# Optimization experiments

Hardware: AMD Instinct MI355X
Metric: run time of the kernel (lower is better)

The kernel has to match this reference:

```python
import jax, jax.numpy as jnp
import numpy as np

B = 4096          # graphs (frames)
NPG = 22          # players per frame
N = B * NPG       # total nodes
E = B * NPG * (NPG - 1)
D_BB = 256        # backbone_dout == GRNN hidden
D_NODE = 128      # raw node feature dim
D_PROJ = 256      # cfg.proj_dout
D_GIN = 64        # glob_din
D_GOUT = 128      # cfg.glob_dout
D_IN = D_BB + D_PROJ  # GRNN input dim = 512


def setup_inputs() -> dict:
    key = jax.random.key(0)
    ks = jax.random.split(key, 24)
    def w(k, shape):
        return jax.random.normal(k, shape, jnp.float32) * 0.05
    inp = {
        "z": jax.random.normal(ks[0], (N, D_BB), jnp.float32),
        "u": jax.random.normal(ks[1], (B, D_GIN), jnp.float32),
        "x": jax.random.normal(ks[2], (N, D_NODE), jnp.float32),
        # edge_index is unused math-wise because GConvGRU is built with K=1 ChebConvs
        "edge_index": jax.random.randint(ks[3], (2, E), 0, N, dtype=jnp.int32),
        "batch": jnp.repeat(jnp.arange(B, dtype=jnp.int32), NPG),
        "batch_size": B,
        "prev_h": jax.random.normal(ks[4], (N, D_BB), jnp.float32),
        # fusion params
        "w_proj": w(ks[5], (D_NODE, D_PROJ)), "b_proj": jnp.zeros((D_PROJ,), jnp.float32),
        "w_glob": w(ks[6], (D_GIN, D_GOUT)), "b_glob": jnp.zeros((D_GOUT,), jnp.float32),
        # GConvGRU (K=1 ChebConv == linear) gate params: update z, reset r, candidate h
        "W_xz": w(ks[7], (D_IN, D_BB)),  "b_xz": jnp.zeros((D_BB,), jnp.float32),
        "W_hz": w(ks[8], (D_BB, D_BB)),  "b_hz": jnp.zeros((D_BB,), jnp.float32),
        "W_xr": w(ks[9], (D_IN, D_BB)),  "b_xr": jnp.zeros((D_BB,), jnp.float32),
        "W_hr": w(ks[10], (D_BB, D_BB)), "b_hr": jnp.zeros((D_BB,), jnp.float32),
        "W_xh": w(ks[11], (D_IN, D_BB)), "b_xh": jnp.zeros((D_BB,), jnp.float32),
        "W_hh": w(ks[12], (D_BB, D_BB)), "b_hh": jnp.zeros((D_BB,), jnp.float32),
    }
    return inp


def reference(z, u, x, edge_index, batch, batch_size, prev_h,
              w_proj, b_proj, w_glob, b_glob,
              W_xz, b_xz, W_hz, b_hz,
              W_xr, b_xr, W_hr, b_hr,
              W_xh, b_xh, W_hh, b_hh):
    # --- GraphGlobalFusion: mean readout + relu(Linear(u)) + concat ---
    sums = jax.ops.segment_sum(z, batch, num_segments=batch_size)            # [B, D_BB]
    cnts = jax.ops.segment_sum(jnp.ones((z.shape[0], 1), z.dtype), batch,
                               num_segments=batch_size)                      # [B, 1]
    graph_emb = sums / jnp.maximum(cnts, 1.0)
    glob_emb = jax.nn.relu(u @ w_glob + b_glob)                              # [B, D_GOUT]
    fused = jnp.concatenate([graph_emb, glob_emb], axis=-1)                  # [B, D_BB+D_GOUT]

    # --- node mode: raw feature projection, then GConvGRU (K=1 -> linear gates) ---
    x_proj = jax.nn.relu(x @ w_proj + b_proj)                                # [N, D_PROJ]
    xin = jnp.concatenate([z, x_proj], axis=-1)                              # [N, D_IN]
    Z = jax.nn.sigmoid(xin @ W_xz + b_xz + prev_h @ W_hz + b_hz)
    R = jax.nn.sigmoid(xin @ W_xr + b_xr + prev_h @ W_hr + b_hr)
    H_tilde = jnp.tanh(xin @ W_xh + b_xh + (prev_h * R) @ W_hh + b_hh)
    h = Z * prev_h + (1.0 - Z) * H_tilde                                     # [N, D_BB]
    return (fused, h)
```

## Files before the change

### kernel.cpp

```cpp
#include <hip/hip_runtime.h>
#include <hip/hip_bf16.h>

#define NNODES 90112
#define BGRAPH 4096
#define NPG 22
#define DBB 256
#define DNODE 128
#define DPROJ 256
#define DGIN 64
#define DGOUT 128

#define WTG_OFF   32768
#define WTHH_OFF  622592
#define WS_BF16_ELEMS 688128

typedef __attribute__((ext_vector_type(8))) short bf16x8;
typedef __attribute__((ext_vector_type(4))) short bf16x4;
typedef __attribute__((ext_vector_type(4))) float f32x4;
typedef __attribute__((ext_vector_type(2))) float f32x2;

__device__ __forceinline__ short f2bf(float f) {
  __hip_bfloat16 h = __float2bfloat16(f);
  return *reinterpret_cast<short*>(&h);
}
__device__ __forceinline__ float bf2f(short s) {
  union { unsigned int u; float f; } c;
  c.u = ((unsigned int)(unsigned short)s) << 16;
  return c.f;
}
__device__ __forceinline__ float fsig(float xv) {
  return __fdividef(1.0f, 1.0f + __expf(-xv));
}
__device__ __forceinline__ float ftanh(float xv) {
  return 1.0f - __fdividef(2.0f, __expf(2.0f * xv) + 1.0f);
}

#define DMA16(gsrc, ldst)                                                        \
  __builtin_amdgcn_global_load_lds(                                              \
      (const __attribute__((address_space(1))) void*)(gsrc),                     \
      (__attribute__((address_space(3))) void*)(ldst), 16, 0, 0)

template<int N>
__device__ __forceinline__ void vmwaitN() {
  static_assert(N >= 0 && N <= 6, "vmcnt range");
  if constexpr (N == 0) asm volatile("s_waitcnt vmcnt(0)" ::: "memory");
  else if constexpr (N == 1) asm volatile("s_waitcnt vmcnt(1)" ::: "memory");
  else if constexpr (N == 2) asm volatile("s_waitcnt vmcnt(2)" ::: "memory");
  else if constexpr (N == 3) asm volatile("s_waitcnt vmcnt(3)" ::: "memory");
  else if constexpr (N == 4) asm volatile("s_waitcnt vmcnt(4)" ::: "memory");
  else if constexpr (N == 5) asm volatile("s_waitcnt vmcnt(5)" ::: "memory");
  else asm volatile("s_waitcnt vmcnt(6)" ::: "memory");
  __builtin_amdgcn_sched_barrier(0);
}
#define LBAR() do { asm volatile("s_waitcnt lgkmcnt(0)" ::: "memory");           \
                    __builtin_amdgcn_s_barrier(); } while (0)

__global__ void pack_weights(const float* __restrict__ w_proj,
                             const float* __restrict__ W_xz, const float* __restrict__ W_hz,
                             const float* __restrict__ W_xr, const float* __restrict__ W_hr,
                             const float* __restrict__ W_xh, const float* __restrict__ W_hh,
                             const float* __restrict__ b_xz, const float* __restrict__ b_hz,
                             const float* __restrict__ b_xr, const float* __restrict__ b_hr,
                             const float* __restrict__ b_xh, const float* __restrict__ b_hh,
                             __hip_bfloat16* __restrict__ wsb, float* __restrict__ wsf) {
  int i = blockIdx.x * 256 + threadIdx.x;
  if (i < 32768) {
    int c = i >> 7, k = i & 127;
    wsb[i] = __float2bfloat16(w_proj[k * DPROJ + c]);
  } else if (i < WTHH_OFF) {
    int j = i - WTG_OFF;
    int kc  = j / 24576;
    int rem = j - kc * 24576;
    int ct  = rem >> 9;
    int q   = rem & 511;
    int l   = q >> 3, e = q & 7;
    int l15 = l & 15, kg = l >> 4;
    int k   = kc * 32 + kg * 8 + e;
    int g   = ct >> 4;
    int c   = (ct & 15) * 16 + l15;
    float v;
    if (g == 0)      v = (k < 512) ? W_xz[k * 256 + c] : W_hz[(k - 512) * 256 + c];
    else if (g == 1) v = (k < 512) ? W_xr[k * 256 + c] : W_hr[(k - 512) * 256 + c];
    else             v = (k < 512) ? W_xh[k * 256 + c] : 0.0f;
    wsb[i] = __float2bfloat16(v);
  } else if (i < WS_BF16_ELEMS) {
    int j = i - WTHH_OFF;
    int kc  = j >> 13;
    int rem = j & 8191;
    int ct  = rem >> 9;
    int q   = rem & 511;
    int l   = q >> 3, e = q & 7;
    int l15 = l & 15, kg = l >> 4;
    int k   = kc * 32 + kg * 8 + e;
    int c   = ct * 16 + l15;
    wsb[i] = __float2bfloat16(W_hh[k * 256 + c]);
  }
  if (i < 256) {
    wsf[i]       = b_xz[i] + b_hz[i];
    wsf[256 + i] = b_xr[i] + b_hr[i];
    wsf[512 + i] = b_xh[i] + b_hh[i];
  }
}

__global__ void fused_head(const float* __restrict__ z, const float* __restrict__ u,
                           const float* __restrict__ w_glob, const float* __restrict__ b_glob,
                           float* __restrict__ out) {
  int b = blockIdx.x;
  int t = threadIdx.x;
  __shared__ float us[DGIN];
  if (t < DGIN) us[t] = u[b * DGIN + t];
  __syncthreads();
  const float* zb = z + (size_t)b * NPG * DBB;
  #pragma unroll
  for (int half = 0; half < 2; ++half) {
    int c = t + half * 128;
    float s = 0.f;
    #pragma unroll
    for (int r = 0; r < NPG; ++r) s += zb[r * DBB + c];
    out[(size_t)b * 384 + c] = s * (1.0f / NPG);
  }
  float acc = b_glob[t];
  #pragma unroll
  for (int k = 0; k < DGIN; ++k) acc += us[k] * w_glob[k * DGOUT + t];
  out[(size_t)b * 384 + 256 + t] = fmaxf(acc, 0.f);
}

#define MFMA16(a, b, c) __builtin_amdgcn_mfma_f32_16x16x32_bf16(a, b, c, 0, 0, 0)

template<int KC>
__device__ __forceinline__ void gstep(
    const float* __restrict__ z, const float* __restrict__ prev_h,
    const __hip_bfloat16* __restrict__ wpk,
    __hip_bfloat16* Wb, __hip_bfloat16* ActC, __hip_bfloat16* XP,
    int tid, int r0, int l15, int lg, int wid, int lane,
    f32x4 (&accz)[4], f32x4 (&accr)[4], f32x4 (&acch)[4]) {
  constexpr int  KN       = KC + 1;
  constexpr bool S        = (KN >= 1 && KN <= 7) || (KN >= 16 && KN <= 23);
  constexpr bool BAR      = (KC >= 1 && KC <= 7) || (KC >= 15 && KC <= 23);
  constexpr bool staged   = (KC < 8) || (KC >= 16);
  constexpr bool has_h    = (KC < 16);
  constexpr int  sB       = (KC < 23) ? ((KN < 16) ? 3 : 2) : 0;
  constexpr int  NW       = sB + (S ? 1 : 0);

  f32x2 sl;
  const int srow = tid >> 4, sc2 = (tid & 15) * 2;
  if constexpr (S) {
    const float* src = (KN < 8) ? z : prev_h;
    constexpr int kofs = (KN < 8 ? KN : KN - 16) * 32;
    sl = *(const f32x2*)(src + (size_t)(r0 + srow) * DBB + kofs + sc2);
  }
  if constexpr (BAR) LBAR();

  bf16x8 act[4];
  #pragma unroll
  for (int rt = 0; rt < 4; ++rt) {
    const int row = rt * 16 + l15;
    if constexpr (staged)
      act[rt] = *(const bf16x8*)&ActC[(KC % 3) * 2560 + row * 40 + lg * 8];
    else {
      const int gk = (KC - 8) * 4 + lg;
      act[rt] = *(const bf16x8*)&XP[row * 256 + ((gk ^ (row & 7)) * 8)];
    }
  }

  vmwaitN<NW>();
  bf16x8 wz = *(const bf16x8*)&Wb[((KC & 1) * 3 + 0) * 8192 + wid * 512 + lane * 8];
  bf16x8 wr = *(const bf16x8*)&Wb[((KC & 1) * 3 + 1) * 8192 + wid * 512 + lane * 8];
  bf16x8 wh;
  if constexpr (has_h)
    wh = *(const bf16x8*)&Wb[((KC & 1) * 3 + 2) * 8192 + wid * 512 + lane * 8];

  __builtin_amdgcn_s_setprio(1);
  #pragma unroll
  for (int rt = 0; rt < 4; ++rt) {
    accz[rt] = MFMA16(wz, act[rt], accz[rt]);
    accr[rt] = MFMA16(wr, act[rt], accr[rt]);
    if constexpr (has_h) acch[rt] = MFMA16(wh, act[rt], acch[rt]);
  }
  __builtin_amdgcn_s_setprio(0);

  if constexpr (KC + 2 <= 23) {
    constexpr int ns = ((KC + 2) < 16) ? 3 : 2;
    #pragma unroll
    for (int g = 0; g < 3; ++g)
      if (g < ns)
        DMA16(wpk + (((size_t)(KC + 2) * 48 + g * 16 + wid) * 64 + lane) * 8,
              Wb + (((KC + 2) & 1) * 3 + g) * 8192 + wid * 512);
  }

  if constexpr (S) {
    unsigned int pk = (unsigned int)(unsigned short)f2bf(sl[0]) |
                      ((unsigned int)(unsigned short)f2bf(sl[1]) << 16);
    *(unsigned int*)&ActC[(KN % 3) * 2560 + srow * 40 + sc2] = pk;
  }
}

template<int S>
__device__ __forceinline__ void hstep(
    const __hip_bfloat16* __restrict__ hpk, __hip_bfloat16* Wb, __hip_bfloat16* XP,
    int l15, int lg, int wid, int lane, f32x4 (&acch)[4]) {
  constexpr int NW = (S <= 5) ? 2 : (S == 6) ? 1 : 0;
  bf16x8 act[4];
  #pragma unroll
  for (int rt = 0; rt < 4; ++rt) {
    const int row = rt * 16 + l15;
    const int gk = S * 4 + lg;
    act[rt] = *(const bf16x8*)&XP[row * 256 + ((gk ^ (row & 7)) * 8)];
  }
  vmwaitN<NW>();
  bf16x8 w = *(const bf16x8*)&Wb[(S % 4) * 8192 + wid * 512 + lane * 8];
  __builtin_amdgcn_s_setprio(1);
  #pragma unroll
  for (int rt = 0; rt < 4; ++rt) acch[rt] = MFMA16(w, act[rt], acch[rt]);
  __builtin_amdgcn_s_setprio(0);
  if constexpr (S + 3 <= 7)
    DMA16(hpk + (((size_t)(S + 3) * 16 + wid) * 64 + lane) * 8,
          Wb + ((S + 3) % 4) * 8192 + wid * 512);
}

__global__ __launch_bounds__(1024, 4)
void grnn_main(const float* __restrict__ z, const float* __restrict__ x,
               const float* __restrict__ prev_h, const float* __restrict__ b_proj,
               const __hip_bfloat16* __restrict__ wsb, const float* __restrict__ wsf,
               float* __restrict__ h_out) {
  __shared__ __align__(16) __hip_bfloat16 Wb[6 * 8192];
  __shared__ __align__(16) __hip_bfloat16 Xs[64 * 128];
  __shared__ __align__(16) __hip_bfloat16 XP[64 * 256];
  __shared__ __align__(16) __hip_bfloat16 ActC[3 * 2560];

  const int r0   = blockIdx.x * 64;
  const int tid  = threadIdx.x;
  const int wid  = tid >> 6;
  const int lane = tid & 63;
  const int l15  = lane & 15;
  const int lg   = lane >> 4;
  const int c0   = wid * 16;
  const int cgrp = (c0 >> 3) + (lg >> 1);
  const int lgl  = (lg & 1) * 4;

  const __hip_bfloat16* wpk = wsb + WTG_OFF;
  const __hip_bfloat16* hpk = wsb + WTHH_OFF;

  {
    int row = tid >> 4, c8 = tid & 15;
    const float* p = x + (size_t)(r0 + row) * DNODE + c8 * 8;
    f32x4 f0 = *(const f32x4*)p;
    f32x4 f1 = *(const f32x4*)(p + 4);
    bf16x8 o;
    o[0]=f2bf(f0[0]); o[1]=f2bf(f0[1]); o[2]=f2bf(f0[2]); o[3]=f2bf(f0[3]);
    o[4]=f2bf(f1[0]); o[5]=f2bf(f1[1]); o[6]=f2bf(f1[2]); o[7]=f2bf(f1[3]);
    *(bf16x8*)&Xs[row * 128 + (c8 ^ (row & 7)) * 8] = o;
  }
  __syncthreads();

  f32x2 sl0;
  {
    int row = tid >> 4, c2 = (tid & 15) * 2;
    sl0 = *(const f32x2*)(z + (size_t)(r0 + row) * DBB + c2);
  }
  f32x4 accp[4] = {};
  {
    const __hip_bfloat16* wp0 = wsb + (size_t)(c0 + l15) * DNODE + lg * 8;
    #pragma unroll
    for (int kb = 0; kb < 4; ++kb) {
      bf16x8 wp = *(const bf16x8*)(wp0 + kb * 32);
      const int gk = kb * 4 + lg;
      bf16x8 act[4];
      #pragma unroll
      for (int rt = 0; rt < 4; ++rt) {
        const int row = rt * 16 + l15;
        act[rt] = *(const bf16x8*)&Xs[row * 128 + (gk ^ (row & 7)) * 8];
      }
      __builtin_amdgcn_s_setprio(1);
      #pragma unroll
      for (int rt = 0; rt < 4; ++rt)
        accp[rt] = MFMA16(wp, act[rt], accp[rt]);
      __builtin_amdgcn_s_setprio(0);
    }
  }
  #pragma unroll
  for (int c = 0; c < 2; ++c)
    #pragma unroll
    for (int g = 0; g < 3; ++g)
      DMA16(wpk + (((size_t)c * 48 + g * 16 + wid) * 64 + lane) * 8,
            Wb + ((c & 1) * 3 + g) * 8192 + wid * 512);
  {
    int row = tid >> 4, c2 = (tid & 15) * 2;
    unsigned int pk = (unsigned int)(unsigned short)f2bf(sl0[0]) |
                      ((unsigned int)(unsigned short)f2bf(sl0[1]) << 16);
    *(unsigned int*)&ActC[0 * 2560 + row * 40 + c2] = pk;
  }
  {
    float4 bp4 = *(const float4*)&b_proj[c0 + lg * 4];
    #pragma unroll
    for (int rt = 0; rt < 4; ++rt) {
      int r = rt * 16 + l15;
      bf16x4 o;
      o[0] = f2bf(fmaxf(accp[rt][0] + bp4.x, 0.f));
      o[1] = f2bf(fmaxf(accp[rt][1] + bp4.y, 0.f));
      o[2] = f2bf(fmaxf(accp[rt][2] + bp4.z, 0.f));
      o[3] = f2bf(fmaxf(accp[rt][3] + bp4.w, 0.f));
      *(bf16x4*)&XP[r * 256 + ((cgrp ^ (r & 7)) * 8) + lgl] = o;
    }
  }
  LBAR();

  f32x4 accz[4] = {}, accr[4] = {}, acch[4] = {};
  #define GS(K) gstep<K>(z, prev_h, wpk, Wb, ActC, XP, tid, r0, l15, lg, wid, lane, accz, accr, acch)
  GS(0);  GS(1);  GS(2);  GS(3);  GS(4);  GS(5);  GS(6);  GS(7);
  GS(8);  GS(9);  GS(10); GS(11); GS(12); GS(13); GS(14); GS(15);
  GS(16); GS(17); GS(18); GS(19); GS(20); GS(21); GS(22); GS(23);
  #undef GS

  #pragma unroll
  for (int s = 0; s < 3; ++s)
    DMA16(hpk + (((size_t)s * 16 + wid) * 64 + lane) * 8, Wb + (s % 4) * 8192 + wid * 512);
  f32x4 phv[4];
  {
    float4 br4 = *(const float4*)&wsf[256 + c0 + lg * 4];
    #pragma unroll
    for (int rt = 0; rt < 4; ++rt) {
      int r = rt * 16 + l15;
      phv[rt] = *(const f32x4*)&prev_h[(size_t)(r0 + r) * DBB + c0 + lg * 4];
      bf16x4 o;
      o[0] = f2bf(phv[rt][0] * fsig(accr[rt][0] + br4.x));
      o[1] = f2bf(phv[rt][1] * fsig(accr[rt][1] + br4.y));
      o[2] = f2bf(phv[rt][2] * fsig(accr[rt][2] + br4.z));
      o[3] = f2bf(phv[rt][3] * fsig(accr[rt][3] + br4.w));
      *(bf16x4*)&XP[r * 256 + ((cgrp ^ (r & 7)) * 8) + lgl] = o;
    }
  }
  LBAR();

  #define HS(S) hstep<S>(hpk, Wb, XP, l15, lg, wid, lane, acch)
  HS(0); HS(1); HS(2); HS(3); HS(4); HS(5); HS(6); HS(7);
  #undef HS

  {
    float4 bz4 = *(const float4*)&wsf[c0 + lg * 4];
    float4 bh4 = *(const float4*)&wsf[512 + c0 + lg * 4];
    #pragma unroll
    for (int rt = 0; rt < 4; ++rt) {
      int r = rt * 16 + l15;
      f32x4 hv;
      float zg = fsig(accz[rt][0] + bz4.x);
      hv[0] = zg * phv[rt][0] + (1.f - zg) * ftanh(acch[rt][0] + bh4.x);
      zg = fsig(accz[rt][1] + bz4.y);
      hv[1] = zg * phv[rt][1] + (1.f - zg) * ftanh(acch[rt][1] + bh4.y);
      zg = fsig(accz[rt][2] + bz4.z);
      hv[2] = zg * phv[rt][2] + (1.f - zg) * ftanh(acch[rt][2] + bh4.z);
      zg = fsig(accz[rt][3] + bz4.w);
      hv[3] = zg * phv[rt][3] + (1.f - zg) * ftanh(acch[rt][3] + bh4.w);
      *(f32x4*)&h_out[(size_t)(r0 + r) * DBB + c0 + lg * 4] = hv;
    }
  }
}

extern "C" void kernel_launch(void* const* d_in, const int* in_sizes, int n_in,
                              void* d_out, int out_size, void* d_ws, size_t ws_size,
                              hipStream_t stream) {
  const float* z      = (const float*)d_in[0];
  const float* u      = (const float*)d_in[1];
  const float* x      = (const float*)d_in[2];
  const float* prev_h = (const float*)d_in[6];
  const float* w_proj = (const float*)d_in[7];
  const float* b_proj = (const float*)d_in[8];
  const float* w_glob = (const float*)d_in[9];
  const float* b_glob = (const float*)d_in[10];
  const float* W_xz   = (const float*)d_in[11];
  const float* b_xz   = (const float*)d_in[12];
  const float* W_hz   = (const float*)d_in[13];
  const float* b_hz   = (const float*)d_in[14];
  const float* W_xr   = (const float*)d_in[15];
  const float* b_xr   = (const float*)d_in[16];
  const float* W_hr   = (const float*)d_in[17];
  const float* b_hr   = (const float*)d_in[18];
  const float* W_xh   = (const float*)d_in[19];
  const float* b_xh   = (const float*)d_in[20];
  const float* W_hh   = (const float*)d_in[21];
  const float* b_hh   = (const float*)d_in[22];

  __hip_bfloat16* wsb = (__hip_bfloat16*)d_ws;
  float* wsf = (float*)((char*)d_ws + (size_t)WS_BF16_ELEMS * 2);

  float* fused = (float*)d_out;
  float* h_out = fused + (size_t)BGRAPH * 384;

  pack_weights<<<dim3(WS_BF16_ELEMS / 256), dim3(256), 0, stream>>>(
      w_proj, W_xz, W_hz, W_xr, W_hr, W_xh, W_hh,
      b_xz, b_hz, b_xr, b_hr, b_xh, b_hh, wsb, wsf);

  fused_head<<<dim3(BGRAPH), dim3(128), 0, stream>>>(z, u, w_glob, b_glob, fused);

  grnn_main<<<dim3(NNODES / 64), dim3(1024), 0, stream>>>(
      z, x, prev_h, b_proj, wsb, wsf, h_out);
}
```

Baseline: 208.2 us.

## Stage full z and prev_h tiles in LDS instead of per-step triple-buffered chunks

Replaces the per-k-step triple-buffered ActC staging of z/prev_h (with a barrier every step) by staging the whole 64x256 z tile into a new LDS buffer up front. prev_h is loaded asynchronously with inline-asm global loads during the x_proj phase of the GEMM and written into the same buffer. This removes most per-step barriers and small loads. The epilogue now reads prev_h from LDS as bf16 rather than re-reading fp32 from global, which lowers the precision of the Z*prev_h blend term. The launch bounds drop the min-blocks hint and LDS usage grows.

```diff
diff --git a/kernel.cpp b/kernel.cpp
--- a/kernel.cpp
+++ b/kernel.cpp
@@ -17,7 +17,6 @@
 typedef __attribute__((ext_vector_type(8))) short bf16x8;
 typedef __attribute__((ext_vector_type(4))) short bf16x4;
 typedef __attribute__((ext_vector_type(4))) float f32x4;
-typedef __attribute__((ext_vector_type(2))) float f32x2;
 
 __device__ __forceinline__ short f2bf(float f) {
   __hip_bfloat16 h = __float2bfloat16(f);
@@ -34,22 +33,33 @@
 __device__ __forceinline__ float ftanh(float xv) {
   return 1.0f - __fdividef(2.0f, __expf(2.0f * xv) + 1.0f);
 }
+__device__ __forceinline__ bf16x8 pack8(f32x4 a, f32x4 b) {
+  bf16x8 o;
+  o[0]=f2bf(a[0]); o[1]=f2bf(a[1]); o[2]=f2bf(a[2]); o[3]=f2bf(a[3]);
+  o[4]=f2bf(b[0]); o[5]=f2bf(b[1]); o[6]=f2bf(b[2]); o[7]=f2bf(b[3]);
+  return o;
+}
 
 #define DMA16(gsrc, ldst)                                                        \
   __builtin_amdgcn_global_load_lds(                                              \
       (const __attribute__((address_space(1))) void*)(gsrc),                     \
       (__attribute__((address_space(3))) void*)(ldst), 16, 0, 0)
 
+#define GLF(dst, p) asm volatile("global_load_dwordx4 %0, %1, off"               \
+                                 : "=&v"(dst) : "v"(p) : "memory")
+
 template<int N>
 __device__ __forceinline__ void vmwaitN() {
-  static_assert(N >= 0 && N <= 6, "vmcnt range");
+  static_assert(N >= 0 && N <= 8, "vmcnt range");
   if constexpr (N == 0) asm volatile("s_waitcnt vmcnt(0)" ::: "memory");
   else if constexpr (N == 1) asm volatile("s_waitcnt vmcnt(1)" ::: "memory");
   else if constexpr (N == 2) asm volatile("s_waitcnt vmcnt(2)" ::: "memory");
   else if constexpr (N == 3) asm volatile("s_waitcnt vmcnt(3)" ::: "memory");
   else if constexpr (N == 4) asm volatile("s_waitcnt vmcnt(4)" ::: "memory");
   else if constexpr (N == 5) asm volatile("s_waitcnt vmcnt(5)" ::: "memory");
-  else asm volatile("s_waitcnt vmcnt(6)" ::: "memory");
+  else if constexpr (N == 6) asm volatile("s_waitcnt vmcnt(6)" ::: "memory");
+  else if constexpr (N == 7) asm volatile("s_waitcnt vmcnt(7)" ::: "memory");
+  else asm volatile("s_waitcnt vmcnt(8)" ::: "memory");
   __builtin_amdgcn_sched_barrier(0);
 }
 #define LBAR() do { asm volatile("s_waitcnt lgkmcnt(0)" ::: "memory");           \
@@ -129,47 +139,29 @@
 
 template<int KC>
 __device__ __forceinline__ void gstep(
-    const float* __restrict__ z, const float* __restrict__ prev_h,
-    const __hip_bfloat16* __restrict__ wpk,
-    __hip_bfloat16* Wb, __hip_bfloat16* ActC, __hip_bfloat16* XP,
-    int tid, int r0, int l15, int lg, int wid, int lane,
+    const __hip_bfloat16* __restrict__ wpk, __hip_bfloat16* Wb,
+    const __hip_bfloat16* Av, const __hip_bfloat16* XP,
+    int l15, int lg, int wid, int lane,
     f32x4 (&accz)[4], f32x4 (&accr)[4], f32x4 (&acch)[4]) {
-  constexpr int  KN       = KC + 1;
-  constexpr bool S        = (KN >= 1 && KN <= 7) || (KN >= 16 && KN <= 23);
-  constexpr bool BAR      = (KC >= 1 && KC <= 7) || (KC >= 15 && KC <= 23);
-  constexpr bool staged   = (KC < 8) || (KC >= 16);
-  constexpr bool has_h    = (KC < 16);
-  constexpr int  sB       = (KC < 23) ? ((KN < 16) ? 3 : 2) : 0;
-  constexpr int  NW       = sB + (S ? 1 : 0);
-
-  f32x2 sl;
-  const int srow = tid >> 4, sc2 = (tid & 15) * 2;
-  if constexpr (S) {
-    const float* src = (KN < 8) ? z : prev_h;
-    constexpr int kofs = (KN < 8 ? KN : KN - 16) * 32;
-    sl = *(const f32x2*)(src + (size_t)(r0 + srow) * DBB + kofs + sc2);
-  }
-  if constexpr (BAR) LBAR();
-
+  constexpr bool has_h = (KC < 16);
+  constexpr int NW = (KC <= 8) ? 3
+                   : (KC == 9 || KC == 10 || KC == 12 || KC == 13) ? 5
+                   : (KC == 11 || KC == 14) ? 3
+                   : (KC <= 22) ? 2 : 0;
+  const __hip_bfloat16* ab = (KC >= 8 && KC < 16) ? XP : Av;
+  const int gk = (KC & 7) * 4 + lg;
   bf16x8 act[4];
   #pragma unroll
   for (int rt = 0; rt < 4; ++rt) {
     const int row = rt * 16 + l15;
-    if constexpr (staged)
-      act[rt] = *(const bf16x8*)&ActC[(KC % 3) * 2560 + row * 40 + lg * 8];
-    else {
-      const int gk = (KC - 8) * 4 + lg;
-      act[rt] = *(const bf16x8*)&XP[row * 256 + ((gk ^ (row & 7)) * 8)];
-    }
-  }
-
+    act[rt] = *(const bf16x8*)(ab + row * 256 + ((gk ^ (row & 7)) * 8));
+  }
   vmwaitN<NW>();
   bf16x8 wz = *(const bf16x8*)&Wb[((KC & 1) * 3 + 0) * 8192 + wid * 512 + lane * 8];
   bf16x8 wr = *(const bf16x8*)&Wb[((KC & 1) * 3 + 1) * 8192 + wid * 512 + lane * 8];
   bf16x8 wh;
   if constexpr (has_h)
     wh = *(const bf16x8*)&Wb[((KC & 1) * 3 + 2) * 8192 + wid * 512 + lane * 8];
-
   __builtin_amdgcn_s_setprio(1);
   #pragma unroll
   for (int rt = 0; rt < 4; ++rt) {
@@ -178,7 +170,6 @@
     if constexpr (has_h) acch[rt] = MFMA16(wh, act[rt], acch[rt]);
   }
   __builtin_amdgcn_s_setprio(0);
-
   if constexpr (KC + 2 <= 23) {
     constexpr int ns = ((KC + 2) < 16) ? 3 : 2;
     #pragma unroll
@@ -186,12 +177,6 @@
       if (g < ns)
         DMA16(wpk + (((size_t)(KC + 2) * 48 + g * 16 + wid) * 64 + lane) * 8,
               Wb + (((KC + 2) & 1) * 3 + g) * 8192 + wid * 512);
-  }
-
-  if constexpr (S) {
-    unsigned int pk = (unsigned int)(unsigned short)f2bf(sl[0]) |
-                      ((unsigned int)(unsigned short)f2bf(sl[1]) << 16);
-    *(unsigned int*)&ActC[(KN % 3) * 2560 + srow * 40 + sc2] = pk;
   }
 }
 
@@ -218,15 +203,14 @@
           Wb + ((S + 3) % 4) * 8192 + wid * 512);
 }
 
-__global__ __launch_bounds__(1024, 4)
+__global__ __launch_bounds__(1024)
 void grnn_main(const float* __restrict__ z, const float* __restrict__ x,
                const float* __restrict__ prev_h, const float* __restrict__ b_proj,
                const __hip_bfloat16* __restrict__ wsb, const float* __restrict__ wsf,
                float* __restrict__ h_out) {
   __shared__ __align__(16) __hip_bfloat16 Wb[6 * 8192];
-  __shared__ __align__(16) __hip_bfloat16 Xs[64 * 128];
+  __shared__ __align__(16) __hip_bfloat16 Av[64 * 256];
   __shared__ __align__(16) __hip_bfloat16 XP[64 * 256];
-  __shared__ __align__(16) __hip_bfloat16 ActC[3 * 2560];
 
   const int r0   = blockIdx.x * 64;
   const int tid  = threadIdx.x;
@@ -237,26 +221,25 @@
   const int c0   = wid * 16;
   const int cgrp = (c0 >> 3) + (lg >> 1);
   const int lgl  = (lg & 1) * 4;
+  const int prow = tid >> 4;
+  const int pg   = tid & 15;
 
   const __hip_bfloat16* wpk = wsb + WTG_OFF;
   const __hip_bfloat16* hpk = wsb + WTHH_OFF;
 
   {
-    int row = tid >> 4, c8 = tid & 15;
-    const float* p = x + (size_t)(r0 + row) * DNODE + c8 * 8;
+    const float* p = x + (size_t)(r0 + prow) * DNODE + pg * 8;
     f32x4 f0 = *(const f32x4*)p;
     f32x4 f1 = *(const f32x4*)(p + 4);
-    bf16x8 o;
-    o[0]=f2bf(f0[0]); o[1]=f2bf(f0[1]); o[2]=f2bf(f0[2]); o[3]=f2bf(f0[3]);
-    o[4]=f2bf(f1[0]); o[5]=f2bf(f1[1]); o[6]=f2bf(f1[2]); o[7]=f2bf(f1[3]);
-    *(bf16x8*)&Xs[row * 128 + (c8 ^ (row & 7)) * 8] = o;
+    *(bf16x8*)&XP[prow * 128 + ((pg ^ (prow & 7)) * 8)] = pack8(f0, f1);
   }
   __syncthreads();
 
-  f32x2 sl0;
-  {
-    int row = tid >> 4, c2 = (tid & 15) * 2;
-    sl0 = *(const f32x2*)(z + (size_t)(r0 + row) * DBB + c2);
+  f32x4 z0, z1, z2, z3;
+  {
+    const float* zb = z + (size_t)(r0 + prow) * DBB + pg * 16;
+    z0 = *(const f32x4*)zb;       z1 = *(const f32x4*)(zb + 4);
+    z2 = *(const f32x4*)(zb + 8); z3 = *(const f32x4*)(zb + 12);
   }
   f32x4 accp[4] = {};
   {
@@ -269,7 +252,7 @@
       #pragma unroll
       for (int rt = 0; rt < 4; ++rt) {
         const int row = rt * 16 + l15;
-        act[rt] = *(const bf16x8*)&Xs[row * 128 + (gk ^ (row & 7)) * 8];
+        act[rt] = *(const bf16x8*)&XP[row * 128 + ((gk ^ (row & 7)) * 8)];
       }
       __builtin_amdgcn_s_setprio(1);
       #pragma unroll
@@ -284,12 +267,7 @@
     for (int g = 0; g < 3; ++g)
       DMA16(wpk + (((size_t)c * 48 + g * 16 + wid) * 64 + lane) * 8,
             Wb + ((c & 1) * 3 + g) * 8192 + wid * 512);
-  {
-    int row = tid >> 4, c2 = (tid & 15) * 2;
-    unsigned int pk = (unsigned int)(unsigned short)f2bf(sl0[0]) |
-                      ((unsigned int)(unsigned short)f2bf(sl0[1]) << 16);
-    *(unsigned int*)&ActC[0 * 2560 + row * 40 + c2] = pk;
-  }
+  LBAR();
   {
     float4 bp4 = *(const float4*)&b_proj[c0 + lg * 4];
     #pragma unroll
@@ -303,31 +281,47 @@
       *(bf16x4*)&XP[r * 256 + ((cgrp ^ (r & 7)) * 8) + lgl] = o;
     }
   }
+  *(bf16x8*)&Av[prow * 256 + (((2 * pg) ^ (prow & 7)) * 8)]     = pack8(z0, z1);
+  *(bf16x8*)&Av[prow * 256 + (((2 * pg + 1) ^ (prow & 7)) * 8)] = pack8(z2, z3);
   LBAR();
 
   f32x4 accz[4] = {}, accr[4] = {}, acch[4] = {};
-  #define GS(K) gstep<K>(z, prev_h, wpk, Wb, ActC, XP, tid, r0, l15, lg, wid, lane, accz, accr, acch)
-  GS(0);  GS(1);  GS(2);  GS(3);  GS(4);  GS(5);  GS(6);  GS(7);
-  GS(8);  GS(9);  GS(10); GS(11); GS(12); GS(13); GS(14); GS(15);
+  const float* phb = prev_h + (size_t)(r0 + prow) * DBB + pg * 8;
+  f32x4 pa0, pa1, pb0, pb1;
+  #define GS(K) gstep<K>(wpk, Wb, Av, XP, l15, lg, wid, lane, accz, accr, acch)
+  GS(0); GS(1); GS(2); GS(3); GS(4); GS(5); GS(6); GS(7);
+  LBAR();
+  GS(8);
+  GLF(pa0, phb); GLF(pa1, phb + 4);
+  GS(9); GS(10);
+  vmwaitN<6>();
+  *(bf16x8*)&Av[prow * 256 + ((pg ^ (prow & 7)) * 8)] = pack8(pa0, pa1);
+  GS(11);
+  GLF(pb0, phb + 128); GLF(pb1, phb + 132);
+  GS(12); GS(13);
+  vmwaitN<6>();
+  *(bf16x8*)&Av[prow * 256 + (((16 + pg) ^ (prow & 7)) * 8)] = pack8(pb0, pb1);
+  GS(14); GS(15);
+  LBAR();
   GS(16); GS(17); GS(18); GS(19); GS(20); GS(21); GS(22); GS(23);
   #undef GS
 
   #pragma unroll
   for (int s = 0; s < 3; ++s)
     DMA16(hpk + (((size_t)s * 16 + wid) * 64 + lane) * 8, Wb + (s % 4) * 8192 + wid * 512);
-  f32x4 phv[4];
   {
     float4 br4 = *(const float4*)&wsf[256 + c0 + lg * 4];
     #pragma unroll
     for (int rt = 0; rt < 4; ++rt) {
       int r = rt * 16 + l15;
-      phv[rt] = *(const f32x4*)&prev_h[(size_t)(r0 + r) * DBB + c0 + lg * 4];
+      int off = r * 256 + ((cgrp ^ (r & 7)) * 8) + lgl;
+      bf16x4 p4 = *(const bf16x4*)&Av[off];
       bf16x4 o;
-      o[0] = f2bf(phv[rt][0] * fsig(accr[rt][0] + br4.x));
-      o[1] = f2bf(phv[rt][1] * fsig(accr[rt][1] + br4.y));
-      o[2] = f2bf(phv[rt][2] * fsig(accr[rt][2] + br4.z));
-      o[3] = f2bf(phv[rt][3] * fsig(accr[rt][3] + br4.w));
-      *(bf16x4*)&XP[r * 256 + ((cgrp ^ (r & 7)) * 8) + lgl] = o;
+      o[0] = f2bf(bf2f(p4[0]) * fsig(accr[rt][0] + br4.x));
+      o[1] = f2bf(bf2f(p4[1]) * fsig(accr[rt][1] + br4.y));
+      o[2] = f2bf(bf2f(p4[2]) * fsig(accr[rt][2] + br4.z));
+      o[3] = f2bf(bf2f(p4[3]) * fsig(accr[rt][3] + br4.w));
+      *(bf16x4*)&XP[off] = o;
     }
   }
   LBAR();
@@ -342,15 +336,16 @@
     #pragma unroll
     for (int rt = 0; rt < 4; ++rt) {
       int r = rt * 16 + l15;
+      bf16x4 p4 = *(const bf16x4*)&Av[r * 256 + ((cgrp ^ (r & 7)) * 8) + lgl];
       f32x4 hv;
       float zg = fsig(accz[rt][0] + bz4.x);
-      hv[0] = zg * phv[rt][0] + (1.f - zg) * ftanh(acch[rt][0] + bh4.x);
+      hv[0] = zg * bf2f(p4[0]) + (1.f - zg) * ftanh(acch[rt][0] + bh4.x);
       zg = fsig(accz[rt][1] + bz4.y);
-      hv[1] = zg * phv[rt][1] + (1.f - zg) * ftanh(acch[rt][1] + bh4.y);
+      hv[1] = zg * bf2f(p4[1]) + (1.f - zg) * ftanh(acch[rt][1] + bh4.y);
       zg = fsig(accz[rt][2] + bz4.z);
-      hv[2] = zg * phv[rt][2] + (1.f - zg) * ftanh(acch[rt][2] + bh4.z);
+      hv[2] = zg * bf2f(p4[2]) + (1.f - zg) * ftanh(acch[rt][2] + bh4.z);
       zg = fsig(accz[rt][3] + bz4.w);
-      hv[3] = zg * phv[rt][3] + (1.f - zg) * ftanh(acch[rt][3] + bh4.w);
+      hv[3] = zg * bf2f(p4[3]) + (1.f - zg) * ftanh(acch[rt][3] + bh4.w);
       *(f32x4*)&h_out[(size_t)(r0 + r) * DBB + c0 + lg * 4] = hv;
     }
   }
```

Result: faster. 195.9 us, median of 3 (-5.9%).
